# Kernel tuning notes

Measured on AMD Instinct MI355X. Metric: run time of the kernel, lower is better.

## Reference

```python
import jax, jax.numpy as jnp
import numpy as np

NUM_HEADS = 3

def setup_inputs() -> dict:
    key = jax.random.key(0)
    k0, k1, k2, k3, k4 = jax.random.split(key, 5)
    B, C, H, W = 2, 96, 64, 64
    N = H * W
    x = jax.random.normal(k0, (B, N, C), jnp.float32)
    # depthwise conv: groups=C, out_channels=3*C -> OIHW weight [3C, 1, 3, 3]
    qkv_w = jax.random.normal(k1, (3 * C, 1, 3, 3), jnp.float32) * 0.1
    qkv_b = jax.random.normal(k2, (3 * C,), jnp.float32) * 0.01
    proj_w = jax.random.normal(k3, (C, C), jnp.float32) * (1.0 / np.sqrt(C))
    proj_b = jax.random.normal(k4, (C,), jnp.float32) * 0.01
    return {"x": x, "qkv_w": qkv_w, "qkv_b": qkv_b,
            "proj_w": proj_w, "proj_b": proj_b, "H": H, "W": W}


def reference(x, qkv_w, qkv_b, proj_w, proj_b, H, W):
    B, N, C = x.shape
    h = NUM_HEADS
    d = C // h
    scale = d ** (-0.5)
    # [B,N,C] -> [B,C,H,W]
    x2d = jnp.transpose(x, (0, 2, 1)).reshape(B, C, H, W)
    # depthwise conv, 'SAME' padding (padding = kernel//2, stride 1)
    qkv = jax.lax.conv_general_dilated(
        x2d, qkv_w, window_strides=(1, 1), padding="SAME",
        feature_group_count=C,
        dimension_numbers=("NCHW", "OIHW", "NCHW"))
    qkv = qkv + qkv_b[None, :, None, None]
    qkv = qkv.reshape(B, 3, h, d, H * W)  # same channel split as torch reshape
    q, k, v = qkv[:, 0], qkv[:, 1], qkv[:, 2]  # each [B,h,d,N]
    # attn = q^T @ k  (q,k permuted to [B,h,N,d] in the original)
    attn = jnp.einsum("bhdn,bhdm->bhnm", q, k) * scale  # [B,h,N,N]
    attn = jax.nn.softmax(attn, axis=-1)
    out = jnp.einsum("bhnm,bhdm->bhnd", attn, v)  # [B,h,N,d]
    # replicate torch: transpose(2,3) -> [B,h,d,N], reshape(B, N, C)
    out = jnp.transpose(out, (0, 1, 3, 2)).reshape(B, H * W, C)
    out = out @ proj_w.T + proj_b
    return out
```

## Files before the change

### kernel.cpp

```cpp
#include <hip/hip_runtime.h>
#include <hip/hip_bf16.h>

typedef short bf16x8 __attribute__((ext_vector_type(8)));
typedef float f32x4 __attribute__((ext_vector_type(4)));
typedef unsigned int u32x4 __attribute__((ext_vector_type(4)));

#define B_ 2
#define C_ 96
#define N_ 4096
#define NH_ 3
#define DH_ 32
#define BH_ 6
#define KSPLIT 8
#define TQB 256
#define MQ 4
#define TK 64
#define WAVES_PER_BLOCK 4
#define KT_PER_BLOCK (N_ / KSPLIT / TK)


__global__ __launch_bounds__(256) void conv_qkv(
    const float* __restrict__ x, const float* __restrict__ qw,
    const float* __restrict__ qb, __hip_bfloat16* __restrict__ q_b,
    __hip_bfloat16* __restrict__ k_b, __hip_bfloat16* __restrict__ vT) {
  __shared__ float xs[18 * 64];
  int b = blockIdx.x / C_;
  int cin = blockIdx.x % C_;
  int y0 = blockIdx.y * 16;
  int yl0 = (y0 == 0) ? 0 : y0 - 1;
  int yl1 = (y0 + 16 > 63) ? 63 : y0 + 16;
  int nload = (yl1 - yl0 + 1) * 64;
  const float* xp = x + (size_t)b * N_ * C_ + cin;
  for (int i = threadIdx.x; i < nload; i += 256)
    xs[i] = xp[(size_t)(yl0 * 64 + i) * C_];
  __syncthreads();

  int s = cin >> 5;
  int cl = cin & 31;
  float w[3][9], bias[3];
#pragma unroll
  for (int r = 0; r < 3; ++r) {
    int o = 3 * cin + r;
#pragma unroll
    for (int t = 0; t < 9; ++t) w[r][t] = qw[o * 9 + t];
    bias[r] = qb[o];
  }
  const float scale = 0.2550349f;
  float mul = (s == 0) ? scale : 1.0f;
  __hip_bfloat16* base_[3];
  int dd_[3];
#pragma unroll
  for (int r = 0; r < 3; ++r) {
    int c = 3 * cl + r, head = c >> 5, dd = c & 31, bh = b * NH_ + head;
    dd_[r] = dd;
    if (s == 2)
      base_[r] = vT + (size_t)bh * N_ * DH_;
    else if (s == 1)
      base_[r] = k_b + (size_t)bh * N_ * DH_;
    else
      base_[r] = q_b + (size_t)bh * N_ * DH_;
  }

  for (int i = threadIdx.x; i < 1024; i += 256) {
    int y = y0 + (i >> 6), xx = i & 63;
    float a0 = bias[0], a1 = bias[1], a2 = bias[2];
#pragma unroll
    for (int dy = 0; dy < 3; ++dy) {
      int ry = y + dy - 1;
      if ((unsigned)ry >= 64u) continue;
#pragma unroll
      for (int dx = 0; dx < 3; ++dx) {
        int rx = xx + dx - 1;
        if ((unsigned)rx >= 64u) continue;
        float xv = xs[(ry - yl0) * 64 + rx];
        a0 += w[0][dy * 3 + dx] * xv;
        a1 += w[1][dy * 3 + dx] * xv;
        a2 += w[2][dy * 3 + dx] * xv;
      }
    }
    int n = y * 64 + xx;
    float av[3] = {a0 * mul, a1 * mul, a2 * mul};
#pragma unroll
    for (int r = 0; r < 3; ++r) {
      int off;
      if (s == 0)
        off = n * DH_ + dd_[r];
      else if (s == 1)
        off = ((n >> 6) << 11) | (((n >> 4) & 3) << 9) | ((n & 15) << 5) | dd_[r];
      else {
        int kap = (((n >> 2) & 3) << 3) | (((n >> 4) & 1) << 2) | (n & 3);
        off = ((n >> 6) << 11) | (((n >> 5) & 1) << 10) | (dd_[r] << 5) | kap;
      }
      base_[r][off] = __float2bfloat16(av[r]);
    }
  }
}

__global__ __launch_bounds__(256, 2) void attn_fwd(
    const __hip_bfloat16* __restrict__ q_b, const __hip_bfloat16* __restrict__ k_b,
    const __hip_bfloat16* __restrict__ vT, float* __restrict__ Opart,
    float* __restrict__ lpart) {
  int qt = blockIdx.x, ks = blockIdx.y, bh = blockIdx.z;
  int tid = threadIdx.x;
  int lane = tid & 63, wave = tid >> 6;
  int c = lane & 15, quad = lane >> 4;

  int q0 = qt * TQB + wave * 64;
  const __hip_bfloat16* qbase = q_b + ((size_t)bh * N_ + q0) * DH_;
  bf16x8 qa[MQ];
#pragma unroll
  for (int m = 0; m < MQ; ++m)
    qa[m] = *(const bf16x8*)(qbase + (m * 16 + c) * DH_ + quad * 8);

  f32x4 oT[2][MQ];
  f32x4 lacT[MQ];
#pragma unroll
  for (int m = 0; m < MQ; ++m) {
    lacT[m] = (f32x4){0.f, 0.f, 0.f, 0.f};
#pragma unroll
    for (int n0 = 0; n0 < 2; ++n0) oT[n0][m] = (f32x4){0.f, 0.f, 0.f, 0.f};
  }
  bf16x8 ones;
  {
    short v = (c == 0) ? (short)0x3F80 : (short)0;
    ones = (bf16x8){v, v, v, v, v, v, v, v};
  }

  const __hip_bfloat16* kb = k_b + (size_t)bh * N_ * DH_;
  const __hip_bfloat16* vb = vT + (size_t)bh * N_ * DH_;
  int key0 = ks * (N_ / KSPLIT);

  bf16x8 kf[2][4];
  {
    size_t tb0 = (size_t)key0 * DH_;
#pragma unroll
    for (int t = 0; t < 4; ++t)
      kf[0][t] = *(const bf16x8*)(kb + tb0 + t * 512 + c * 32 + quad * 8);
  }

#pragma unroll
  for (int kt = 0; kt < KT_PER_BLOCK; ++kt) {
    const int cur = kt & 1, nxt = cur ^ 1;
    size_t tbase = (size_t)(key0 + kt * TK) * DH_;

    if (kt + 1 < KT_PER_BLOCK) {
      size_t tnext = (size_t)(key0 + (kt + 1) * TK) * DH_;
#pragma unroll
      for (int t = 0; t < 4; ++t)
        kf[nxt][t] = *(const bf16x8*)(kb + tnext + t * 512 + c * 32 + quad * 8);
    }

    bf16x8 vf[2][2];
#pragma unroll
    for (int n0 = 0; n0 < 2; ++n0)
#pragma unroll
      for (int h = 0; h < 2; ++h)
        vf[n0][h] = *(const bf16x8*)(vb + tbase + h * 1024 + (n0 * 16 + c) * 32 + quad * 8);

#pragma unroll
    for (int m = 0; m < MQ; ++m) {
      f32x4 pT[4];
      f32x4 z = {0.f, 0.f, 0.f, 0.f};
#pragma unroll
      for (int t = 0; t < 4; ++t)
        pT[t] = __builtin_amdgcn_mfma_f32_16x16x32_bf16(kf[cur][t], qa[m], z, 0, 0, 0);

#pragma unroll
      for (int t = 0; t < 4; ++t)
#pragma unroll
        for (int r = 0; r < 4; ++r)
          pT[t][r] = __builtin_amdgcn_exp2f(pT[t][r]);

      unsigned wv[4][2];
#pragma unroll
      for (int t = 0; t < 4; ++t) {
        unsigned h0 = __builtin_bit_cast(unsigned short, __float2bfloat16(pT[t][0]));
        unsigned h1 = __builtin_bit_cast(unsigned short, __float2bfloat16(pT[t][1]));
        unsigned h2 = __builtin_bit_cast(unsigned short, __float2bfloat16(pT[t][2]));
        unsigned h3 = __builtin_bit_cast(unsigned short, __float2bfloat16(pT[t][3]));
        wv[t][0] = h0 | (h1 << 16);
        wv[t][1] = h2 | (h3 << 16);
      }
#pragma unroll
      for (int h = 0; h < 2; ++h) {
        u32x4 bw = {wv[2 * h][0], wv[2 * h][1], wv[2 * h + 1][0], wv[2 * h + 1][1]};
        bf16x8 pB = __builtin_bit_cast(bf16x8, bw);
        oT[0][m] = __builtin_amdgcn_mfma_f32_16x16x32_bf16(vf[0][h], pB, oT[0][m], 0, 0, 0);
        oT[1][m] = __builtin_amdgcn_mfma_f32_16x16x32_bf16(vf[1][h], pB, oT[1][m], 0, 0, 0);
        lacT[m] = __builtin_amdgcn_mfma_f32_16x16x32_bf16(ones, pB, lacT[m], 0, 0, 0);
      }
    }
  }

  float* Ob = Opart + (size_t)(ks * BH_ + bh) * DH_ * N_ + q0;
#pragma unroll
  for (int n0 = 0; n0 < 2; ++n0)
#pragma unroll
    for (int m = 0; m < MQ; ++m)
#pragma unroll
      for (int r = 0; r < 4; ++r)
        Ob[(size_t)(n0 * 16 + quad * 4 + r) * N_ + m * 16 + c] = oT[n0][m][r];
  if (lane < 16) {
    float* lb = lpart + (size_t)(ks * BH_ + bh) * N_ + q0;
#pragma unroll
    for (int m = 0; m < MQ; ++m) lb[m * 16 + lane] = lacT[m][0];
  }
}

__global__ __launch_bounds__(256) void proj_out(
    const float* __restrict__ Opart, const float* __restrict__ lpart,
    const float* __restrict__ pw, const float* __restrict__ pb,
    float* __restrict__ out) {
  __shared__ float Wt[C_][100];
  __shared__ float Pt[16][100];
  __shared__ float bias[C_];
  int tid = threadIdx.x;
  for (int i = tid; i < C_ * C_; i += 256) Wt[i / C_][i % C_] = pw[i];
  if (tid < C_) bias[tid] = pb[tid];
  int row0 = blockIdx.x * 16;
  for (int i = tid; i < 16 * C_; i += 256) {
    int r = i / C_, cc = i % C_;
    int g = row0 + r;
    int b = g >> 12;
    int f = (g & 4095) * C_ + cc;
    int hh = f >> 17;
    int n = f & 4095;
    float osum = 0.f, lsum = 0.f;
    size_t obase = (size_t)g * C_ + cc;
    size_t lbase = (size_t)(b * NH_ + hh) * N_ + n;
#pragma unroll
    for (int ksq = 0; ksq < KSPLIT; ++ksq) {
      osum += Opart[(size_t)ksq * (BH_ * DH_ * N_) + obase];
      lsum += lpart[(size_t)ksq * (BH_ * N_) + lbase];
    }
    Pt[r][cc] = osum / lsum;
  }
  __syncthreads();

  int row = tid >> 4, cg = tid & 15;
  float acc[6] = {};
  for (int kk = 0; kk < C_; kk += 4) {
    f32x4 pv = *(const f32x4*)&Pt[row][kk];
    f32x4 wv[6];
#pragma unroll
    for (int i2 = 0; i2 < 6; ++i2) wv[i2] = *(const f32x4*)&Wt[cg * 6 + i2][kk];
#pragma unroll
    for (int i2 = 0; i2 < 6; ++i2)
      acc[i2] += pv[0] * wv[i2][0] + pv[1] * wv[i2][1] +
                 pv[2] * wv[i2][2] + pv[3] * wv[i2][3];
  }
#pragma unroll
  for (int i2 = 0; i2 < 6; ++i2)
    out[(size_t)(row0 + row) * C_ + cg * 6 + i2] = acc[i2] + bias[cg * 6 + i2];
}

extern "C" void kernel_launch(void* const* d_in, const int* in_sizes, int n_in,
                              void* d_out, int out_size, void* d_ws, size_t ws_size,
                              hipStream_t stream) {
  const float* x = (const float*)d_in[0];
  const float* qw = (const float*)d_in[1];
  const float* qb = (const float*)d_in[2];
  const float* pw = (const float*)d_in[3];
  const float* pb = (const float*)d_in[4];

  char* ws = (char*)d_ws;
  __hip_bfloat16* q_b = (__hip_bfloat16*)(ws);
  __hip_bfloat16* k_b = (__hip_bfloat16*)(ws + 1572864);
  __hip_bfloat16* vT = (__hip_bfloat16*)(ws + 3145728);
  float* Opart = (float*)(ws + 4718592);
  float* lpart = (float*)(ws + 29884416);

  hipLaunchKernelGGL(conv_qkv, dim3(B_ * C_, 4), dim3(256), 0, stream, x, qw, qb, q_b, k_b, vT);
  hipLaunchKernelGGL(attn_fwd, dim3(N_ / TQB, KSPLIT, BH_), dim3(256), 0, stream,
                     q_b, k_b, vT, Opart, lpart);
  hipLaunchKernelGGL(proj_out, dim3((B_ * N_) / 16, 1), dim3(256), 0, stream,
                     Opart, lpart, pw, pb, (float*)d_out);
}
```

Baseline: 123.9 us.

## Stage K/V tiles in swizzled shared memory and halve key split

Each block now loads the K and V tiles cooperatively into double-buffered LDS with an XOR swizzle, instead of every wave reading K/V fragments from global memory separately. The four waves share each tile, which cuts redundant global and L2 traffic, at the cost of a barrier per key tile. KSPLIT also drops from 8 to 4, halving the partial-output workspace and the reduction work in proj_out, while leaving fewer blocks (384) to fill the GPU.

```diff
diff --git a/kernel.cpp b/kernel.cpp
--- a/kernel.cpp
+++ b/kernel.cpp
@@ -11,7 +11,7 @@
 #define NH_ 3
 #define DH_ 32
 #define BH_ 6
-#define KSPLIT 8
+#define KSPLIT 4
 #define TQB 256
 #define MQ 4
 #define TK 64
@@ -96,10 +96,13 @@
   }
 }
 
+__device__ __forceinline__ int swz(int a) { return a ^ (((a >> 6) & 7) << 4); }
+
 __global__ __launch_bounds__(256, 2) void attn_fwd(
     const __hip_bfloat16* __restrict__ q_b, const __hip_bfloat16* __restrict__ k_b,
     const __hip_bfloat16* __restrict__ vT, float* __restrict__ Opart,
     float* __restrict__ lpart) {
+  __shared__ __align__(16) unsigned char smem[2][8192];
   int qt = blockIdx.x, ks = blockIdx.y, bh = blockIdx.z;
   int tid = threadIdx.x;
   int lane = tid & 63, wave = tid >> 6;
@@ -126,36 +129,48 @@
     ones = (bf16x8){v, v, v, v, v, v, v, v};
   }
 
-  const __hip_bfloat16* kb = k_b + (size_t)bh * N_ * DH_;
-  const __hip_bfloat16* vb = vT + (size_t)bh * N_ * DH_;
+  const unsigned char* kbb = (const unsigned char*)(k_b + (size_t)bh * N_ * DH_);
+  const unsigned char* vbb = (const unsigned char*)(vT + (size_t)bh * N_ * DH_);
   int key0 = ks * (N_ / KSPLIT);
 
-  bf16x8 kf[2][4];
+  int rk[4], rv[2][2];
+#pragma unroll
+  for (int t = 0; t < 4; ++t) rk[t] = swz(t * 1024 + c * 64 + quad * 16);
+#pragma unroll
+  for (int n0 = 0; n0 < 2; ++n0)
+#pragma unroll
+    for (int h = 0; h < 2; ++h)
+      rv[n0][h] = 4096 + swz(h * 2048 + (n0 * 16 + c) * 64 + quad * 16);
+  int sdst = swz(tid * 16);
+
   {
-    size_t tb0 = (size_t)key0 * DH_;
-#pragma unroll
-    for (int t = 0; t < 4; ++t)
-      kf[0][t] = *(const bf16x8*)(kb + tb0 + t * 512 + c * 32 + quad * 8);
-  }
+    size_t tb = (size_t)(key0) * 64;
+    u32x4 kreg = *(const u32x4*)(kbb + tb + tid * 16);
+    u32x4 vreg = *(const u32x4*)(vbb + tb + tid * 16);
+    *(u32x4*)(smem[0] + sdst) = kreg;
+    *(u32x4*)(smem[0] + 4096 + sdst) = vreg;
+  }
+  __syncthreads();
 
 #pragma unroll
   for (int kt = 0; kt < KT_PER_BLOCK; ++kt) {
     const int cur = kt & 1, nxt = cur ^ 1;
-    size_t tbase = (size_t)(key0 + kt * TK) * DH_;
-
+
+    u32x4 kreg, vreg;
     if (kt + 1 < KT_PER_BLOCK) {
-      size_t tnext = (size_t)(key0 + (kt + 1) * TK) * DH_;
-#pragma unroll
-      for (int t = 0; t < 4; ++t)
-        kf[nxt][t] = *(const bf16x8*)(kb + tnext + t * 512 + c * 32 + quad * 8);
-    }
-
-    bf16x8 vf[2][2];
+      size_t tn = (size_t)(key0 + (kt + 1) * TK) * 64;
+      kreg = *(const u32x4*)(kbb + tn + tid * 16);
+      vreg = *(const u32x4*)(vbb + tn + tid * 16);
+    }
+
+    const unsigned char* sb = smem[cur];
+    bf16x8 kf[4], vf[2][2];
+#pragma unroll
+    for (int t = 0; t < 4; ++t) kf[t] = *(const bf16x8*)(sb + rk[t]);
 #pragma unroll
     for (int n0 = 0; n0 < 2; ++n0)
 #pragma unroll
-      for (int h = 0; h < 2; ++h)
-        vf[n0][h] = *(const bf16x8*)(vb + tbase + h * 1024 + (n0 * 16 + c) * 32 + quad * 8);
+      for (int h = 0; h < 2; ++h) vf[n0][h] = *(const bf16x8*)(sb + rv[n0][h]);
 
 #pragma unroll
     for (int m = 0; m < MQ; ++m) {
@@ -163,7 +178,7 @@
       f32x4 z = {0.f, 0.f, 0.f, 0.f};
 #pragma unroll
       for (int t = 0; t < 4; ++t)
-        pT[t] = __builtin_amdgcn_mfma_f32_16x16x32_bf16(kf[cur][t], qa[m], z, 0, 0, 0);
+        pT[t] = __builtin_amdgcn_mfma_f32_16x16x32_bf16(kf[t], qa[m], z, 0, 0, 0);
 
 #pragma unroll
       for (int t = 0; t < 4; ++t)
@@ -190,6 +205,12 @@
         lacT[m] = __builtin_amdgcn_mfma_f32_16x16x32_bf16(ones, pB, lacT[m], 0, 0, 0);
       }
     }
+
+    if (kt + 1 < KT_PER_BLOCK) {
+      *(u32x4*)(smem[nxt] + sdst) = kreg;
+      *(u32x4*)(smem[nxt] + 4096 + sdst) = vreg;
+    }
+    __syncthreads();
   }
 
   float* Ob = Opart + (size_t)(ks * BH_ + bh) * DH_ * N_ + q0;
@@ -268,7 +289,7 @@
   __hip_bfloat16* k_b = (__hip_bfloat16*)(ws + 1572864);
   __hip_bfloat16* vT = (__hip_bfloat16*)(ws + 3145728);
   float* Opart = (float*)(ws + 4718592);
-  float* lpart = (float*)(ws + 29884416);
+  float* lpart = (float*)(ws + 17301504);
 
   hipLaunchKernelGGL(conv_qkv, dim3(B_ * C_, 4), dim3(256), 0, stream, x, qw, qb, q_b, k_b, vT);
   hipLaunchKernelGGL(attn_fwd, dim3(N_ / TQB, KSPLIT, BH_), dim3(256), 0, stream,
```

Measured after the change: 129.7 us. 4.7% more time.
